# Optimization experiments

Hardware: AMD Instinct MI355X
Metric: run time of the kernel (lower is better)

The kernel has to match this reference:

```python
import jax, jax.numpy as jnp
import numpy as np

N_NODES = 50000
N_EDGES = 600000
NUM_ENTITIES = 50000
EMBED = 128
HIDDEN = 128
NUM_TYPES = 16


def setup_inputs() -> dict:
    key = jax.random.key(0)
    ks = jax.random.split(key, 12)
    entity = jax.random.randint(ks[0], (N_NODES,), 0, NUM_ENTITIES, dtype=jnp.int64 if jax.config.jax_enable_x64 else jnp.int32)
    edge_index = jax.random.randint(ks[1], (2, N_EDGES), 0, N_NODES, dtype=jnp.int32)
    s = 1.0 / np.sqrt(EMBED)
    emb = jax.random.normal(ks[2], (NUM_ENTITIES, EMBED), jnp.float32)
    emb = emb.at[0].set(0.0)  # padding_idx=0
    W1_l = jax.random.uniform(ks[3], (EMBED, HIDDEN), jnp.float32, -s, s)
    b1 = jax.random.uniform(ks[4], (HIDDEN,), jnp.float32, -s, s)
    W1_r = jax.random.uniform(ks[5], (EMBED, HIDDEN), jnp.float32, -s, s)
    W2_l = jax.random.uniform(ks[6], (HIDDEN, HIDDEN), jnp.float32, -s, s)
    b2 = jax.random.uniform(ks[7], (HIDDEN,), jnp.float32, -s, s)
    W2_r = jax.random.uniform(ks[8], (HIDDEN, HIDDEN), jnp.float32, -s, s)
    Wc = jax.random.uniform(ks[9], (HIDDEN, NUM_TYPES), jnp.float32, -s, s)
    bc = jax.random.uniform(ks[10], (NUM_TYPES,), jnp.float32, -s, s)
    return {"entity": entity, "edge_index": edge_index, "emb": emb,
            "W1_l": W1_l, "b1": b1, "W1_r": W1_r,
            "W2_l": W2_l, "b2": b2, "W2_r": W2_r,
            "Wc": Wc, "bc": bc}


def _sage_conv(x, src, dst, Wl, bl, Wr):
    # PyG SAGEConv (aggr='mean'): out = lin_l(mean_{j->i} x_j) + lin_r(x_i)
    msgs = x[src]                                            # [E, D] gather
    agg = jax.ops.segment_sum(msgs, dst, num_segments=N_NODES)
    deg = jax.ops.segment_sum(jnp.ones((src.shape[0],), x.dtype), dst, num_segments=N_NODES)
    agg = agg / jnp.maximum(deg, 1.0)[:, None]               # mean; 0 for isolated nodes
    return agg @ Wl + bl + x @ Wr


def reference(entity, edge_index, emb, W1_l, b1, W1_r, W2_l, b2, W2_r, Wc, bc):
    src, dst = edge_index[0], edge_index[1]
    x = emb[entity]                                          # [N, 128] embedding lookup
    x = jax.nn.relu(_sage_conv(x, src, dst, W1_l, b1, W1_r))
    x = _sage_conv(x, src, dst, W2_l, b2, W2_r)
    return x @ Wc + bc                                       # [N, num_node_types]
```

## Files before the change

### kernel.cpp

```cpp
#include <hip/hip_runtime.h>

typedef _Float16 half4  __attribute__((ext_vector_type(4)));
typedef _Float16 half8  __attribute__((ext_vector_type(8)));
typedef float    f32x4  __attribute__((ext_vector_type(4)));

#define EC 768
#define CAP 4096
#define CHUNK 1536

__device__ __forceinline__ void gather_dev(const int* __restrict__ ent,
                                           const float* __restrict__ emb,
                                           _Float16* __restrict__ X, int gb, int N) {
  int t = gb * 256 + threadIdx.x;
  if (t >= N * 16) return;
  int node = t >> 4, g = t & 15;
  const float4* s = (const float4*)(emb + (long)ent[node] * 128 + g * 8);
  float4 a = s[0], c = s[1];
  half8 o;
  o[0] = (_Float16)a.x; o[1] = (_Float16)a.y; o[2] = (_Float16)a.z; o[3] = (_Float16)a.w;
  o[4] = (_Float16)c.x; o[5] = (_Float16)c.y; o[6] = (_Float16)c.z; o[7] = (_Float16)c.w;
  *(half8*)(X + (long)t * 8) = o;
}

__device__ __forceinline__ void pack_dev(const float* Wa, const float* Wb,
                                         _Float16* out, int NT, int ncols, int t) {
  int lane = t & 63, tile = t >> 6;
  int nt = tile % NT, kt = tile / NT;
  int n  = nt * 16 + (lane & 15);
  int kb = kt * 32 + (lane >> 4) * 8;
  half8 o;
#pragma unroll
  for (int j = 0; j < 8; ++j) {
    int k = kb + j;
    float w = (k < 128) ? Wa[k * ncols + n] : Wb[(k - 128) * ncols + n];
    o[j] = (_Float16)w;
  }
  *(half8*)(out + (long)t * 8) = o;
}

__global__ __launch_bounds__(256) void bucketA_k(
    const int* __restrict__ src, const int* __restrict__ dst,
    int* __restrict__ cur, int* __restrict__ buck,
    const int* __restrict__ ent, const float* __restrict__ emb, _Float16* __restrict__ X,
    const float* __restrict__ W1l, const float* __restrict__ W1r, _Float16* __restrict__ Wp1,
    const float* __restrict__ W2l, const float* __restrict__ W2r, const float* __restrict__ Wc,
    _Float16* __restrict__ Wz, const float* __restrict__ b2, const float* __restrict__ bc,
    float* __restrict__ bpr, int N, int E, int NA, int NBUCK, int ST, int IBA) {
  int b = blockIdx.x;
  if (b < IBA) {
    int grp = b / ST, ph = b % ST;
    if (ph != 0) { gather_dev(ent, emb, X, grp * (ST - 1) + ph - 1, N); return; }
    __shared__ int lbin[256], gbase[256];
    int tl = threadIdx.x;
    lbin[tl] = 0; __syncthreads();
    int e0 = grp * CHUNK;
    int pk[6], bn[6], lr[6];
#pragma unroll
    for (int k = 0; k < 6; ++k) {
      int e = e0 + k * 256 + tl;
      bn[k] = -1;
      if (e < E) {
        int d = dst[e];
        bn[k] = d >> 8;
        pk[k] = (src[e] << 8) | (d & 255);
        lr[k] = atomicAdd(&lbin[bn[k]], 1);
      }
    }
    __syncthreads();
    gbase[tl] = (tl < NBUCK && lbin[tl]) ? atomicAdd(&cur[tl], lbin[tl]) : 0;
    __syncthreads();
#pragma unroll
    for (int k = 0; k < 6; ++k) {
      if (bn[k] >= 0) {
        int idx = gbase[bn[k]] + lr[k];
        if (idx < CAP) buck[(long)bn[k] * CAP + idx] = pk[k];
      }
    }
  } else if (b < IBA + 16) {
    pack_dev(W1l, W1r, Wp1, 8, 128, (b - IBA) * 256 + threadIdx.x);
  } else if (b < IBA + 32) {
    int i = (b - IBA - 16) * 256 + threadIdx.x;
    int j = i & 7, lane = (i >> 3) & 63, tile = i >> 9;
    int nt = tile & 1, kt = tile >> 1;
    int k = kt * 32 + (lane >> 4) * 8 + j;
    int c = lane & 15;
    const float* W = nt ? W2r : W2l;
    float s = 0.f;
#pragma unroll 8
    for (int q = 0; q < 128; ++q) s += W[k * 128 + q] * Wc[q * 16 + c];
    Wz[i] = (_Float16)s;
  } else {
    int n = threadIdx.x;
    if (n < 16) {
      float s = bc[n];
      for (int k = 0; k < 128; ++k) s += b2[k] * Wc[k * 16 + n];
      bpr[n] = s;
    }
  }
}

__global__ __launch_bounds__(256) void bucketB_k(
    const int* __restrict__ cur, const int* __restrict__ buck,
    int* __restrict__ row_off, int* __restrict__ csr, int N, int E, int NBUCK) {
  int B0 = blockIdx.x, tl = threadIdx.x;
  __shared__ int sA[256], cnt[256], sB[256], run[256];
  sA[tl] = (tl < NBUCK) ? cur[tl] : 0; __syncthreads();
  for (int off = 1; off < 256; off <<= 1) {
    int a = sA[tl], bb = (tl >= off) ? sA[tl - off] : 0;
    __syncthreads(); sA[tl] = a + bb; __syncthreads();
  }
  int bsz = cur[B0]; if (bsz > CAP) bsz = CAP;
  int ebase = sA[B0] - bsz;
  cnt[tl] = 0; __syncthreads();
  const int* bp = buck + (long)B0 * CAP;
  for (int i = tl; i < bsz; i += 256) atomicAdd(&cnt[bp[i] & 255], 1);
  __syncthreads();
  int cv = cnt[tl];
  sB[tl] = cv; __syncthreads();
  for (int off = 1; off < 256; off <<= 1) {
    int a = sB[tl], bb = (tl >= off) ? sB[tl - off] : 0;
    __syncthreads(); sB[tl] = a + bb; __syncthreads();
  }
  int loff = sB[tl] - cv;
  int node = (B0 << 8) + tl;
  if (node < N) row_off[node] = ebase + loff;
  if (B0 == 0 && tl == 0) row_off[N] = E;
  run[tl] = loff; __syncthreads();
  for (int i = tl; i < bsz; i += 256) {
    int w = bp[i];
    int r = atomicAdd(&run[w & 255], 1);
    csr[ebase + r] = w >> 8;
  }
}

__device__ __forceinline__ void agg_to_lds(const _Float16* __restrict__ X,
                                           const int* __restrict__ row_off,
                                           const int* __restrict__ csr,
                                           _Float16* ab, int* eidx,
                                           int row0, int M, int lane) {
  int nd_end = min(row0 + 16, M);
  int ebeg = row_off[row0 < M ? row0 : M - 1];
  int eend = row_off[nd_end];
  int cnt  = eend - ebeg;
  bool fits = (cnt <= EC);
  if (fits)
    for (int i = lane; i < cnt; i += 64) eidx[i] = csr[ebeg + i];
  int g = lane >> 4, j = lane & 15;
#pragma unroll
  for (int batch = 0; batch < 4; ++batch) {
    int node = row0 + batch * 4 + g;
    int nc = (node < M) ? node : M - 1;
    int beg = row_off[nc], end = row_off[nc + 1];
    half8 acc = (half8)(_Float16)0.f;
    if (fits) {
      const int* ix = eidx + (beg - ebeg);
      int n = end - beg;
#pragma unroll 8
      for (int e = 0; e < n; ++e) {
        half8 v = *(const half8*)(X + (long)ix[e] * 128 + j * 8);
        acc += v;
      }
    } else {
#pragma unroll 8
      for (int e = beg; e < end; ++e) {
        half8 v = *(const half8*)(X + (long)csr[e] * 128 + j * 8);
        acc += v;
      }
    }
    _Float16 inv = (_Float16)(1.f / fmaxf((float)(end - beg), 1.f));
    acc *= (half8)inv;
    *(half8*)(ab + (batch * 4 + g) * 136 + j * 8) = acc;
  }
}

__global__ __launch_bounds__(128) void gemm1z_k(const _Float16* __restrict__ X,
                                                const int* __restrict__ row_off,
                                                const int* __restrict__ csr,
                                                const _Float16* __restrict__ Bp,
                                                const float* __restrict__ bias,
                                                const _Float16* __restrict__ Bz,
                                                const float* __restrict__ bprime,
                                                _Float16* __restrict__ Zl,
                                                float* __restrict__ Pr, int M) {
  __shared__ _Float16 abuf[2][16 * 136];
  __shared__ int      ebuf[2][EC];
  int wave = threadIdx.x >> 6, lane = threadIdx.x & 63;
  _Float16* ab = abuf[wave];
  int row0 = blockIdx.x * 32 + wave * 16;
  agg_to_lds(X, row_off, csr, ab, ebuf[wave], row0, M, lane);
  int m = lane & 15, quad = lane >> 4;
  int arow = row0 + m; if (arow > M - 1) arow = M - 1;
  f32x4 acc[8];
#pragma unroll
  for (int i = 0; i < 8; ++i) acc[i] = (f32x4){0.f, 0.f, 0.f, 0.f};
#pragma unroll
  for (int kt = 0; kt < 8; ++kt) {
    half8 af = (kt < 4) ? *(const half8*)(ab + m * 136 + kt * 32 + quad * 8)
                        : *(const half8*)(X + (long)arow * 128 + (kt - 4) * 32 + quad * 8);
#pragma unroll
    for (int nt = 0; nt < 8; ++nt) {
      half8 bf = *(const half8*)(Bp + ((long)(kt * 8 + nt) * 64 + lane) * 8);
      acc[nt] = __builtin_amdgcn_mfma_f32_16x16x32_f16(af, bf, acc[nt], 0, 0, 0);
    }
  }
#pragma unroll
  for (int nt = 0; nt < 8; ++nt) {
    float bv = bias[nt * 16 + m];
#pragma unroll
    for (int r = 0; r < 4; ++r)
      ab[(quad * 4 + r) * 136 + nt * 16 + m] = (_Float16)fmaxf(acc[nt][r] + bv, 0.f);
  }
  f32x4 a0 = (f32x4){0.f, 0.f, 0.f, 0.f}, a1 = a0;
#pragma unroll
  for (int kt = 0; kt < 4; ++kt) {
    half8 af = *(const half8*)(ab + m * 136 + kt * 32 + quad * 8);
    half8 b0 = *(const half8*)(Bz + ((long)(kt * 2 + 0) * 64 + lane) * 8);
    half8 b1 = *(const half8*)(Bz + ((long)(kt * 2 + 1) * 64 + lane) * 8);
    a0 = __builtin_amdgcn_mfma_f32_16x16x32_f16(af, b0, a0, 0, 0, 0);
    a1 = __builtin_amdgcn_mfma_f32_16x16x32_f16(af, b1, a1, 0, 0, 0);
  }
  float bv = bprime[m];
#pragma unroll
  for (int r = 0; r < 4; ++r) {
    int orow = row0 + quad * 4 + r;
    if (orow < M) {
      Zl[(long)orow * 16 + m] = (_Float16)a0[r];
      Pr[(long)orow * 16 + m] = a1[r] + bv;
    }
  }
}

__global__ __launch_bounds__(256) void aggout_k(const _Float16* __restrict__ Zl,
                                                const float* __restrict__ Pr,
                                                const int* __restrict__ row_off,
                                                const int* __restrict__ csr,
                                                float* __restrict__ out, int M) {
  int t = blockIdx.x * 256 + threadIdx.x;
  int node = t >> 2, q = t & 3;
  if (node >= M) return;
  int beg = row_off[node], end = row_off[node + 1];
  float a0 = 0.f, a1 = 0.f, a2 = 0.f, a3 = 0.f;
#pragma unroll 8
  for (int e = beg; e < end; ++e) {
    half4 v = *(const half4*)(Zl + (long)csr[e] * 16 + q * 4);
    a0 += (float)v[0]; a1 += (float)v[1]; a2 += (float)v[2]; a3 += (float)v[3];
  }
  float inv = 1.f / fmaxf((float)(end - beg), 1.f);
  long o = (long)node * 16 + q * 4;
  const float4 pv = *(const float4*)(Pr + o);
  float4 ov;
  ov.x = a0 * inv + pv.x; ov.y = a1 * inv + pv.y;
  ov.z = a2 * inv + pv.z; ov.w = a3 * inv + pv.w;
  *(float4*)(out + o) = ov;
}

extern "C" void kernel_launch(void* const* d_in, const int* in_sizes, int n_in,
                              void* d_out, int out_size, void* d_ws, size_t ws_size,
                              hipStream_t stream) {
  const int N = in_sizes[0];
  const int E = in_sizes[1] / 2;
  const int*   entity = (const int*)d_in[0];
  const int*   e_src  = (const int*)d_in[1];
  const int*   e_dst  = e_src + E;
  const float* emb    = (const float*)d_in[2];
  const float* W1l    = (const float*)d_in[3];
  const float* b1     = (const float*)d_in[4];
  const float* W1r    = (const float*)d_in[5];
  const float* W2l    = (const float*)d_in[6];
  const float* b2     = (const float*)d_in[7];
  const float* W2r    = (const float*)d_in[8];
  const float* Wc     = (const float*)d_in[9];
  const float* bc     = (const float*)d_in[10];
  float* out = (float*)d_out;

  const int NBUCK = (N + 255) >> 8;

  char* p = (char*)d_ws;
  _Float16* x0  = (_Float16*)p; p += (size_t)N * 128 * 2;
  _Float16* Wp1 = (_Float16*)p; p += 256 * 128 * 2;
  _Float16* Wz  = (_Float16*)p; p += 128 * 32 * 2;
  float*    bpr = (float*)p;    p += 16 * 4;
  _Float16* Zl  = (_Float16*)p; p += (size_t)N * 16 * 2;
  float*    Pr  = (float*)p;    p += (size_t)N * 16 * 4;
  int* cur     = (int*)p; p += (size_t)NBUCK * 4;
  int* row_off = (int*)p; p += (size_t)(N + 1) * 4;
  int* csr     = (int*)p; p += (size_t)E * 4;
  int* buck    = (int*)p; p += (size_t)NBUCK * CAP * 4;

  const int NA = (E + CHUNK - 1) / CHUNK;
  const int GB = (N * 16 + 255) / 256;
  const int GAper = (GB + NA - 1) / NA;
  const int ST  = GAper + 1;
  const int IBA = ST * NA;

  hipMemsetAsync(cur, 0, (size_t)NBUCK * 4, stream);

  bucketA_k<<<IBA + 33, 256, 0, stream>>>(e_src, e_dst, cur, buck,
                                          entity, emb, x0, W1l, W1r, Wp1,
                                          W2l, W2r, Wc, Wz, b2, bc, bpr,
                                          N, E, NA, NBUCK, ST, IBA);
  bucketB_k<<<NBUCK, 256, 0, stream>>>(cur, buck, row_off, csr, N, E, NBUCK);
  gemm1z_k<<<(N + 31) / 32, 128, 0, stream>>>(x0, row_off, csr, Wp1, b1,
                                              Wz, bpr, Zl, Pr, N);
  aggout_k<<<(N * 4 + 255) / 256, 256, 0, stream>>>(Zl, Pr, row_off, csr, out, N);
}
```

Before: 160.1 us.

## Split neighbor edges across lanes with shuffle reduction and pad bucket counters

In both gather-aggregation stages, neighbors of a node are now split across 4 lane groups: 4 lane groups per node in the first layer's aggregation, 16 threads per node in the final one. Partial sums are combined with cross-lane shuffles, which is meant to shorten the serial per-node latency chain and expose more concurrent loads. The global bucket counters are padded to separate 64-byte slots to avoid atomic contention on shared cache lines. In exchange it adds shuffle work and idle lanes for low-degree nodes, and layer 1 now walks nodes one at a time instead of four in parallel.

New measurement: 168.6 us. 1.05x slower.

```diff
diff --git a/kernel.cpp b/kernel.cpp
--- a/kernel.cpp
+++ b/kernel.cpp
@@ -7,6 +7,14 @@
 #define EC 768
 #define CAP 4096
 #define CHUNK 1536
+#define CPAD 16
+
+__device__ __forceinline__ half8 shfl_xor_h8(half8 v, int m) {
+  union { half8 h; int i[4]; } u; u.h = v;
+#pragma unroll
+  for (int k = 0; k < 4; ++k) u.i[k] = __shfl_xor(u.i[k], m, 64);
+  return u.h;
+}
 
 __device__ __forceinline__ void gather_dev(const int* __restrict__ ent,
                                            const float* __restrict__ emb,
@@ -67,7 +75,7 @@
       }
     }
     __syncthreads();
-    gbase[tl] = (tl < NBUCK && lbin[tl]) ? atomicAdd(&cur[tl], lbin[tl]) : 0;
+    gbase[tl] = (tl < NBUCK && lbin[tl]) ? atomicAdd(&cur[tl * CPAD], lbin[tl]) : 0;
     __syncthreads();
 #pragma unroll
     for (int k = 0; k < 6; ++k) {
@@ -104,12 +112,12 @@
     int* __restrict__ row_off, int* __restrict__ csr, int N, int E, int NBUCK) {
   int B0 = blockIdx.x, tl = threadIdx.x;
   __shared__ int sA[256], cnt[256], sB[256], run[256];
-  sA[tl] = (tl < NBUCK) ? cur[tl] : 0; __syncthreads();
+  sA[tl] = (tl < NBUCK) ? cur[tl * CPAD] : 0; __syncthreads();
   for (int off = 1; off < 256; off <<= 1) {
     int a = sA[tl], bb = (tl >= off) ? sA[tl - off] : 0;
     __syncthreads(); sA[tl] = a + bb; __syncthreads();
   }
-  int bsz = cur[B0]; if (bsz > CAP) bsz = CAP;
+  int bsz = cur[B0 * CPAD]; if (bsz > CAP) bsz = CAP;
   int ebase = sA[B0] - bsz;
   cnt[tl] = 0; __syncthreads();
   const int* bp = buck + (long)B0 * CAP;
@@ -146,30 +154,30 @@
   if (fits)
     for (int i = lane; i < cnt; i += 64) eidx[i] = csr[ebeg + i];
   int g = lane >> 4, j = lane & 15;
-#pragma unroll
-  for (int batch = 0; batch < 4; ++batch) {
-    int node = row0 + batch * 4 + g;
+#pragma unroll 2
+  for (int n = 0; n < 16; ++n) {
+    int node = row0 + n;
     int nc = (node < M) ? node : M - 1;
     int beg = row_off[nc], end = row_off[nc + 1];
+    int d = end - beg;
     half8 acc = (half8)(_Float16)0.f;
     if (fits) {
       const int* ix = eidx + (beg - ebeg);
-      int n = end - beg;
-#pragma unroll 8
-      for (int e = 0; e < n; ++e) {
+      for (int e = g; e < d; e += 4) {
         half8 v = *(const half8*)(X + (long)ix[e] * 128 + j * 8);
         acc += v;
       }
     } else {
-#pragma unroll 8
-      for (int e = beg; e < end; ++e) {
-        half8 v = *(const half8*)(X + (long)csr[e] * 128 + j * 8);
+      for (int e = g; e < d; e += 4) {
+        half8 v = *(const half8*)(X + (long)csr[beg + e] * 128 + j * 8);
         acc += v;
       }
     }
-    _Float16 inv = (_Float16)(1.f / fmaxf((float)(end - beg), 1.f));
+    acc += shfl_xor_h8(acc, 16);
+    acc += shfl_xor_h8(acc, 32);
+    _Float16 inv = (_Float16)(1.f / fmaxf((float)d, 1.f));
     acc *= (half8)inv;
-    *(half8*)(ab + (batch * 4 + g) * 136 + j * 8) = acc;
+    if (g == 0) *(half8*)(ab + n * 136 + j * 8) = acc;
   }
 }
 
@@ -236,22 +244,29 @@
                                                 const int* __restrict__ csr,
                                                 float* __restrict__ out, int M) {
   int t = blockIdx.x * 256 + threadIdx.x;
-  int node = t >> 2, q = t & 3;
+  int node = t >> 4;
   if (node >= M) return;
+  int sub = t & 15, es = sub >> 2, q = sub & 3;
   int beg = row_off[node], end = row_off[node + 1];
   float a0 = 0.f, a1 = 0.f, a2 = 0.f, a3 = 0.f;
-#pragma unroll 8
-  for (int e = beg; e < end; ++e) {
+#pragma unroll 4
+  for (int e = beg + es; e < end; e += 4) {
     half4 v = *(const half4*)(Zl + (long)csr[e] * 16 + q * 4);
     a0 += (float)v[0]; a1 += (float)v[1]; a2 += (float)v[2]; a3 += (float)v[3];
   }
-  float inv = 1.f / fmaxf((float)(end - beg), 1.f);
-  long o = (long)node * 16 + q * 4;
-  const float4 pv = *(const float4*)(Pr + o);
-  float4 ov;
-  ov.x = a0 * inv + pv.x; ov.y = a1 * inv + pv.y;
-  ov.z = a2 * inv + pv.z; ov.w = a3 * inv + pv.w;
-  *(float4*)(out + o) = ov;
+  a0 += __shfl_xor(a0, 4, 64); a1 += __shfl_xor(a1, 4, 64);
+  a2 += __shfl_xor(a2, 4, 64); a3 += __shfl_xor(a3, 4, 64);
+  a0 += __shfl_xor(a0, 8, 64); a1 += __shfl_xor(a1, 8, 64);
+  a2 += __shfl_xor(a2, 8, 64); a3 += __shfl_xor(a3, 8, 64);
+  if (es == 0) {
+    float inv = 1.f / fmaxf((float)(end - beg), 1.f);
+    long o = (long)node * 16 + q * 4;
+    const float4 pv = *(const float4*)(Pr + o);
+    float4 ov;
+    ov.x = a0 * inv + pv.x; ov.y = a1 * inv + pv.y;
+    ov.z = a2 * inv + pv.z; ov.w = a3 * inv + pv.w;
+    *(float4*)(out + o) = ov;
+  }
 }
 
 extern "C" void kernel_launch(void* const* d_in, const int* in_sizes, int n_in,
@@ -282,7 +297,7 @@
   float*    bpr = (float*)p;    p += 16 * 4;
   _Float16* Zl  = (_Float16*)p; p += (size_t)N * 16 * 2;
   float*    Pr  = (float*)p;    p += (size_t)N * 16 * 4;
-  int* cur     = (int*)p; p += (size_t)NBUCK * 4;
+  int* cur     = (int*)p; p += (size_t)NBUCK * CPAD * 4;
   int* row_off = (int*)p; p += (size_t)(N + 1) * 4;
   int* csr     = (int*)p; p += (size_t)E * 4;
   int* buck    = (int*)p; p += (size_t)NBUCK * CAP * 4;
@@ -293,7 +308,7 @@
   const int ST  = GAper + 1;
   const int IBA = ST * NA;
 
-  hipMemsetAsync(cur, 0, (size_t)NBUCK * 4, stream);
+  hipMemsetAsync(cur, 0, (size_t)NBUCK * CPAD * 4, stream);
 
   bucketA_k<<<IBA + 33, 256, 0, stream>>>(e_src, e_dst, cur, buck,
                                           entity, emb, x0, W1l, W1r, Wp1,
@@ -302,5 +317,5 @@
   bucketB_k<<<NBUCK, 256, 0, stream>>>(cur, buck, row_off, csr, N, E, NBUCK);
   gemm1z_k<<<(N + 31) / 32, 128, 0, stream>>>(x0, row_off, csr, Wp1, b1,
                                               Wz, bpr, Zl, Pr, N);
-  aggout_k<<<(N * 4 + 255) / 256, 256, 0, stream>>>(Zl, Pr, row_off, csr, out, N);
-}
+  aggout_k<<<(N * 16 + 255) / 256, 256, 0, stream>>>(Zl, Pr, row_off, csr, out, N);
+}
```
